# Kernel optimization log

Measured on AMD Instinct MI355X. Metric: run time of the kernel, lower is better.

The kernel has to match this reference:

```python
import jax, jax.numpy as jnp
import numpy as np

NUM_USERS = 100000
NUM_ITEMS = 100000
D = 64
L = 3
B = 4096
K = 50


def setup_inputs() -> dict:
    key = jax.random.key(0)
    ks = jax.random.split(key, 8)
    user_ids = jax.random.randint(ks[0], (B,), 0, NUM_USERS)
    item_ids = jax.random.randint(ks[1], (B,), 0, NUM_ITEMS)
    social_neighbors = jax.random.randint(ks[2], (B, K), 0, NUM_USERS)
    attention_mask = jax.random.uniform(ks[3], (B, K), dtype=jnp.float32)
    user_table = jax.random.normal(ks[4], (NUM_USERS, D), dtype=jnp.float32) * 0.1
    item_table = jax.random.normal(ks[5], (NUM_ITEMS, D), dtype=jnp.float32) * 0.1
    # xavier-ish scale for the square Linear layers
    Ws = jax.random.normal(ks[6], (L, D, D), dtype=jnp.float32) * (1.0 / np.sqrt(D))
    bs = jnp.zeros((L, D), dtype=jnp.float32)
    return {
        "user_ids": user_ids,
        "item_ids": item_ids,
        "social_neighbors": social_neighbors,
        "attention_mask": attention_mask,
        "user_table": user_table,
        "item_table": item_table,
        "Ws": Ws,
        "bs": bs,
    }


def reference(user_ids, item_ids, social_neighbors, attention_mask,
              user_table, item_table, Ws, bs):
    user_emb = user_table[user_ids]            # [B, D]
    item_emb = item_table[item_ids]            # [B, D]
    neighbor_emb = user_table[social_neighbors]  # [B, K, D]
    mask = attention_mask[..., None]           # [B, K, 1]
    for l in range(Ws.shape[0]):
        # faithful to original: mask is re-applied to neighbor_emb every layer
        neighbor_emb = neighbor_emb * mask
        neighbor_info = jnp.mean(neighbor_emb, axis=1)  # [B, D]
        # nn.Linear: x @ W.T + b
        user_emb = jax.nn.relu((user_emb + neighbor_info) @ Ws[l].T + bs[l])
    scores = user_emb @ item_emb.T              # [B, B]
    return scores
```

## Files before the change

### kernel.cpp

```cpp
#include <hip/hip_runtime.h>

#define BATCH 4096
#define DIM 64
#define KN 50
#define NL 3

__global__ __launch_bounds__(256) void rows_kernel(
    const int* __restrict__ user_ids,
    const int* __restrict__ item_ids,
    const int* __restrict__ nbrs,
    const float* __restrict__ mask,
    const float* __restrict__ user_table,
    const float* __restrict__ item_table,
    const float* __restrict__ Ws,
    const float* __restrict__ bs,
    float* __restrict__ Uout,
    float* __restrict__ Iout)
{
    __shared__ float Wlds[NL * 64 * 65];
    __shared__ float blds[NL * 64];
    __shared__ float xbuf[4][64];

    const int tid = threadIdx.x;

    for (int idx = tid; idx < NL * 64 * 64; idx += 256) {
        const int l = idx >> 12;
        const int rem = idx & 4095;
        const int j = rem >> 6;
        const int i = rem & 63;
        Wlds[l * (64 * 65) + j * 65 + i] = Ws[idx];
    }
    if (tid < NL * 64) blds[tid] = bs[tid];
    __syncthreads();

    const int wave = tid >> 6;
    const int lane = tid & 63;
    const int b = (blockIdx.x << 2) + wave;

    const int it = item_ids[b];
    Iout[b * DIM + lane] = item_table[it * DIM + lane];

    const int u = user_ids[b];
    float x = user_table[u * DIM + lane];

    int ni = 0;
    float wi = 0.0f;
    if (lane < KN) {
        ni = nbrs[b * KN + lane];
        wi = mask[b * KN + lane];
    }

    float acc1 = 0.f, acc2 = 0.f, acc3 = 0.f;
    #pragma unroll
    for (int k = 0; k < KN; ++k) {
        const int nk = __shfl(ni, k);
        const float wk = __shfl(wi, k);
        const float v = user_table[nk * DIM + lane];
        const float w2 = wk * wk;
        acc1 = fmaf(wk, v, acc1);
        acc2 = fmaf(w2, v, acc2);
        acc3 = fmaf(w2 * wk, v, acc3);
    }
    const float inv = 1.0f / (float)KN;
    float nm0 = acc1 * inv, nm1 = acc2 * inv, nm2 = acc3 * inv;

    #pragma unroll
    for (int l = 0; l < NL; ++l) {
        const float nm = (l == 0) ? nm0 : (l == 1) ? nm1 : nm2;
        const float t = x + nm;
        __syncthreads();
        xbuf[wave][lane] = t;
        __syncthreads();
        float y = blds[l * 64 + lane];
        const float* wrow = &Wlds[l * (64 * 65) + lane * 65];
        #pragma unroll
        for (int i = 0; i < 64; ++i)
            y = fmaf(wrow[i], xbuf[wave][i], y);
        x = fmaxf(y, 0.0f);
    }
    Uout[b * DIM + lane] = x;
}

__global__ __launch_bounds__(256) void scores_kernel(
    const float* __restrict__ U,
    const float* __restrict__ V,
    float* __restrict__ C)
{
    __shared__ float Ut[64 * 128];
    __shared__ float Vt[64 * 128];

    const int tid = threadIdx.x;
    const int rowBase = blockIdx.y << 7;
    const int colBase = blockIdx.x << 7;

    const float4* U4 = (const float4*)(U + (size_t)rowBase * DIM);
    const float4* V4 = (const float4*)(V + (size_t)colBase * DIM);
    #pragma unroll
    for (int c = 0; c < 8; ++c) {
        const int flat = (c << 8) + tid;
        const int row = flat >> 4;
        const int cv = flat & 15;
        const float4 uv = U4[flat];
        const float4 vv = V4[flat];
        const int k0 = cv << 2;
        Ut[(k0 + 0) * 128 + row] = uv.x;
        Ut[(k0 + 1) * 128 + row] = uv.y;
        Ut[(k0 + 2) * 128 + row] = uv.z;
        Ut[(k0 + 3) * 128 + row] = uv.w;
        Vt[(k0 + 0) * 128 + row] = vv.x;
        Vt[(k0 + 1) * 128 + row] = vv.y;
        Vt[(k0 + 2) * 128 + row] = vv.z;
        Vt[(k0 + 3) * 128 + row] = vv.w;
    }
    __syncthreads();

    const int tx = tid & 15;
    const int ty = tid >> 4;

    float acc[8][8];
    #pragma unroll
    for (int i = 0; i < 8; ++i)
        #pragma unroll
        for (int j = 0; j < 8; ++j)
            acc[i][j] = 0.0f;

    #pragma unroll 4
    for (int k = 0; k < 64; ++k) {
        const float4 a0 = *(const float4*)&Ut[k * 128 + ty * 8];
        const float4 a1 = *(const float4*)&Ut[k * 128 + ty * 8 + 4];
        const float4 b0 = *(const float4*)&Vt[k * 128 + tx * 8];
        const float4 b1 = *(const float4*)&Vt[k * 128 + tx * 8 + 4];
        const float a[8] = {a0.x, a0.y, a0.z, a0.w, a1.x, a1.y, a1.z, a1.w};
        const float bb[8] = {b0.x, b0.y, b0.z, b0.w, b1.x, b1.y, b1.z, b1.w};
        #pragma unroll
        for (int i = 0; i < 8; ++i)
            #pragma unroll
            for (int j = 0; j < 8; ++j)
                acc[i][j] = fmaf(a[i], bb[j], acc[i][j]);
    }

    #pragma unroll
    for (int i = 0; i < 8; ++i) {
        float* crow = C + (size_t)(rowBase + ty * 8 + i) * BATCH + colBase + tx * 8;
        *(float4*)(crow + 0) = make_float4(acc[i][0], acc[i][1], acc[i][2], acc[i][3]);
        *(float4*)(crow + 4) = make_float4(acc[i][4], acc[i][5], acc[i][6], acc[i][7]);
    }
}

extern "C" void kernel_launch(void* const* d_in, const int* in_sizes, int n_in,
                              void* d_out, int out_size, void* d_ws, size_t ws_size,
                              hipStream_t stream)
{
    const int* user_ids   = (const int*)d_in[0];
    const int* item_ids   = (const int*)d_in[1];
    const int* nbrs       = (const int*)d_in[2];
    const float* mask     = (const float*)d_in[3];
    const float* utable   = (const float*)d_in[4];
    const float* itable   = (const float*)d_in[5];
    const float* Ws       = (const float*)d_in[6];
    const float* bs       = (const float*)d_in[7];
    float* out = (float*)d_out;

    float* U = (float*)d_ws;
    float* I = U + BATCH * DIM;

    rows_kernel<<<BATCH / 4, 256, 0, stream>>>(user_ids, item_ids, nbrs, mask,
                                               utable, itable, Ws, bs, U, I);
    scores_kernel<<<dim3(32, 32), 256, 0, stream>>>(U, I, out);
}
```

Before: 162.3 us.

## Use bf16 MFMA for the scores GEMM and drop the per-layer barriers

The row kernel now writes the user and item embeddings as bf16. The scores kernel is replaced with one that has no shared memory: each wave loads 16-row bf16 A fragments directly and runs two 16x16x32 bf16 MFMA instructions per 16x16 output tile over 16 column tiles. The block-wide __syncthreads around the per-wave xbuf in the MLP layers is removed, relying on wave-synchronous execution. This aims to cut scores-kernel ALU time and LDS transposes. In exchange it loses precision from bf16 rounding, and each lane's output is stored as a scalar, giving narrower 64-byte row segments.

```diff
diff --git a/kernel.cpp b/kernel.cpp
--- a/kernel.cpp
+++ b/kernel.cpp
@@ -1,9 +1,13 @@
 #include <hip/hip_runtime.h>
+#include <hip/hip_bf16.h>
 
 #define BATCH 4096
 #define DIM 64
 #define KN 50
 #define NL 3
+
+typedef __attribute__((ext_vector_type(8))) short short8;
+typedef __attribute__((ext_vector_type(4))) float f32x4;
 
 __global__ __launch_bounds__(256) void rows_kernel(
     const int* __restrict__ user_ids,
@@ -14,8 +18,8 @@
     const float* __restrict__ item_table,
     const float* __restrict__ Ws,
     const float* __restrict__ bs,
-    float* __restrict__ Uout,
-    float* __restrict__ Iout)
+    __hip_bfloat16* __restrict__ Uout,
+    __hip_bfloat16* __restrict__ Iout)
 {
     __shared__ float Wlds[NL * 64 * 65];
     __shared__ float blds[NL * 64];
@@ -38,7 +42,7 @@
     const int b = (blockIdx.x << 2) + wave;
 
     const int it = item_ids[b];
-    Iout[b * DIM + lane] = item_table[it * DIM + lane];
+    Iout[b * DIM + lane] = __float2bfloat16(item_table[it * DIM + lane]);
 
     const int u = user_ids[b];
     float x = user_table[u * DIM + lane];
@@ -62,15 +66,12 @@
         acc3 = fmaf(w2 * wk, v, acc3);
     }
     const float inv = 1.0f / (float)KN;
-    float nm0 = acc1 * inv, nm1 = acc2 * inv, nm2 = acc3 * inv;
+    const float nm0 = acc1 * inv, nm1 = acc2 * inv, nm2 = acc3 * inv;
 
     #pragma unroll
     for (int l = 0; l < NL; ++l) {
         const float nm = (l == 0) ? nm0 : (l == 1) ? nm1 : nm2;
-        const float t = x + nm;
-        __syncthreads();
-        xbuf[wave][lane] = t;
-        __syncthreads();
+        xbuf[wave][lane] = x + nm;
         float y = blds[l * 64 + lane];
         const float* wrow = &Wlds[l * (64 * 65) + lane * 65];
         #pragma unroll
@@ -78,72 +79,43 @@
             y = fmaf(wrow[i], xbuf[wave][i], y);
         x = fmaxf(y, 0.0f);
     }
-    Uout[b * DIM + lane] = x;
+    Uout[b * DIM + lane] = __float2bfloat16(x);
 }
 
 __global__ __launch_bounds__(256) void scores_kernel(
-    const float* __restrict__ U,
-    const float* __restrict__ V,
+    const __hip_bfloat16* __restrict__ U,
+    const __hip_bfloat16* __restrict__ V,
     float* __restrict__ C)
 {
-    __shared__ float Ut[64 * 128];
-    __shared__ float Vt[64 * 128];
+    const int tid = threadIdx.x;
+    const int wave = tid >> 6;
+    const int lane = tid & 63;
+    const int quad = lane >> 4;
+    const int l16 = lane & 15;
 
-    const int tid = threadIdx.x;
-    const int rowBase = blockIdx.y << 7;
-    const int colBase = blockIdx.x << 7;
+    const int row0 = (blockIdx.y << 6) + (wave << 4);
+    const int colG = blockIdx.x << 8;
 
-    const float4* U4 = (const float4*)(U + (size_t)rowBase * DIM);
-    const float4* V4 = (const float4*)(V + (size_t)colBase * DIM);
-    #pragma unroll
-    for (int c = 0; c < 8; ++c) {
-        const int flat = (c << 8) + tid;
-        const int row = flat >> 4;
-        const int cv = flat & 15;
-        const float4 uv = U4[flat];
-        const float4 vv = V4[flat];
-        const int k0 = cv << 2;
-        Ut[(k0 + 0) * 128 + row] = uv.x;
-        Ut[(k0 + 1) * 128 + row] = uv.y;
-        Ut[(k0 + 2) * 128 + row] = uv.z;
-        Ut[(k0 + 3) * 128 + row] = uv.w;
-        Vt[(k0 + 0) * 128 + row] = vv.x;
-        Vt[(k0 + 1) * 128 + row] = vv.y;
-        Vt[(k0 + 2) * 128 + row] = vv.z;
-        Vt[(k0 + 3) * 128 + row] = vv.w;
-    }
-    __syncthreads();
+    const short* Us = (const short*)U;
+    const short* Vs = (const short*)V;
 
-    const int tx = tid & 15;
-    const int ty = tid >> 4;
-
-    float acc[8][8];
-    #pragma unroll
-    for (int i = 0; i < 8; ++i)
-        #pragma unroll
-        for (int j = 0; j < 8; ++j)
-            acc[i][j] = 0.0f;
+    const short* ap = Us + (row0 + l16) * DIM + quad * 8;
+    const short8 a0 = *(const short8*)(ap);
+    const short8 a1 = *(const short8*)(ap + 32);
 
     #pragma unroll 4
-    for (int k = 0; k < 64; ++k) {
-        const float4 a0 = *(const float4*)&Ut[k * 128 + ty * 8];
-        const float4 a1 = *(const float4*)&Ut[k * 128 + ty * 8 + 4];
-        const float4 b0 = *(const float4*)&Vt[k * 128 + tx * 8];
-        const float4 b1 = *(const float4*)&Vt[k * 128 + tx * 8 + 4];
-        const float a[8] = {a0.x, a0.y, a0.z, a0.w, a1.x, a1.y, a1.z, a1.w};
-        const float bb[8] = {b0.x, b0.y, b0.z, b0.w, b1.x, b1.y, b1.z, b1.w};
+    for (int ct = 0; ct < 16; ++ct) {
+        const int col0 = colG + (ct << 4);
+        const short* bp = Vs + (col0 + l16) * DIM + quad * 8;
+        const short8 b0 = *(const short8*)(bp);
+        const short8 b1 = *(const short8*)(bp + 32);
+        f32x4 acc = {0.f, 0.f, 0.f, 0.f};
+        acc = __builtin_amdgcn_mfma_f32_16x16x32_bf16(a0, b0, acc, 0, 0, 0);
+        acc = __builtin_amdgcn_mfma_f32_16x16x32_bf16(a1, b1, acc, 0, 0, 0);
+        float* cp = C + (size_t)(row0 + (quad << 2)) * BATCH + col0 + l16;
         #pragma unroll
-        for (int i = 0; i < 8; ++i)
-            #pragma unroll
-            for (int j = 0; j < 8; ++j)
-                acc[i][j] = fmaf(a[i], bb[j], acc[i][j]);
-    }
-
-    #pragma unroll
-    for (int i = 0; i < 8; ++i) {
-        float* crow = C + (size_t)(rowBase + ty * 8 + i) * BATCH + colBase + tx * 8;
-        *(float4*)(crow + 0) = make_float4(acc[i][0], acc[i][1], acc[i][2], acc[i][3]);
-        *(float4*)(crow + 4) = make_float4(acc[i][4], acc[i][5], acc[i][6], acc[i][7]);
+        for (int r = 0; r < 4; ++r)
+            cp[(size_t)r * BATCH] = acc[r];
     }
 }
 
@@ -161,10 +133,10 @@
     const float* bs       = (const float*)d_in[7];
     float* out = (float*)d_out;
 
-    float* U = (float*)d_ws;
-    float* I = U + BATCH * DIM;
+    __hip_bfloat16* Ubf = (__hip_bfloat16*)d_ws;
+    __hip_bfloat16* Ibf = Ubf + BATCH * DIM;
 
     rows_kernel<<<BATCH / 4, 256, 0, stream>>>(user_ids, item_ids, nbrs, mask,
-                                               utable, itable, Ws, bs, U, I);
-    scores_kernel<<<dim3(32, 32), 256, 0, stream>>>(U, I, out);
+                                               utable, itable, Ws, bs, Ubf, Ibf);
+    scores_kernel<<<dim3(16, 64), 256, 0, stream>>>(Ubf, Ibf, out);
 }
```

New measurement: 141.7 us. 12.7% less time.
